# Performance work log

Measured on AMD Instinct MI355X. Metric: run time of the kernel, lower is better.

The kernel has to match this reference:

```python
import jax, jax.numpy as jnp
import numpy as np

B, N, C = 16, 2048, 256  # dim=256, hidden_dim=2*dim -> v,gate each width C
LN_EPS = 1e-5


def setup_inputs() -> dict:
    key = jax.random.key(0)
    ks = jax.random.split(key, 6)
    std = 0.02
    return {
        "x": jax.random.normal(ks[0], (B, N, C), dtype=jnp.float32),
        "H": 64,
        "W": 32,
        "ln_w": jnp.ones((C,), jnp.float32),
        "ln_b": jnp.zeros((C,), jnp.float32),
        "w_hidden": jax.random.normal(ks[1], (C, 2 * C), jnp.float32) * std,
        "b_hidden": jnp.zeros((2 * C,), jnp.float32),
        "w_kv": jax.random.normal(ks[2], (C, C), jnp.float32) * std,  # qkv_bias=False
        "gamma": jnp.ones((2, C), jnp.float32),   # torch.ones(2, dim)
        "beta": jnp.zeros((2, C), jnp.float32),   # torch.zeros(2, dim)
        "w_proj": jax.random.normal(ks[3], (C, C), jnp.float32) * std,
        "b_proj": jnp.zeros((C,), jnp.float32),
    }


def reference(x, H, W, ln_w, ln_b, w_hidden, b_hidden, w_kv, gamma, beta, w_proj, b_proj):
    # H, W are unused by the original forward (pos conv is dead code).
    b, n, c = x.shape
    # LayerNorm
    mu = jnp.mean(x, axis=-1, keepdims=True)
    var = jnp.mean(jnp.square(x - mu), axis=-1, keepdims=True)
    normed = (x - mu) * jax.lax.rsqrt(var + LN_EPS) * ln_w + ln_b
    # to_hidden: Linear + SiLU, then chunk into v, gate (each width c)
    h = jax.nn.silu(normed @ w_hidden + b_hidden)
    v, gate = h[..., :c], h[..., c:]
    # kv projection, then offset-scale into q, k
    Z = normed @ w_kv                                  # (b, n, c)
    QK = Z[..., None, :] * gamma + beta                # (b, n, 2, c)
    q, k = QK[..., 0, :], QK[..., 1, :]
    # relu^2 quadratic attention (no softmax)
    attn = jnp.einsum('bid,bjd->bij', q, k) / n        # (b, n, n)
    A = jnp.square(jax.nn.relu(attn))
    V = jnp.einsum('bij,bjd->bid', A, v)               # (b, n, c)
    # SiLU gating, output projection, residual
    out = (V * gate) @ w_proj + b_proj
    return out + x
```

## Files before the change

kernel.cpp:

```cpp
#include <hip/hip_runtime.h>

#define BN 32768
#define NB 16
#define NN 2048
#define CC 256
#define JT 64
#define NTILES (NN / JT)

using short8  = __attribute__((ext_vector_type(8))) short;
using floatx4 = __attribute__((ext_vector_type(4))) float;

__device__ __forceinline__ unsigned short f2bf(float f) {
  unsigned u = __builtin_bit_cast(unsigned, f);
  u += 0x7fffu + ((u >> 16) & 1u);
  return (unsigned short)(u >> 16);
}
__device__ __forceinline__ float bf2f(unsigned short h) {
  unsigned u = ((unsigned)h) << 16;
  return __builtin_bit_cast(float, u);
}
__device__ __forceinline__ unsigned pk4fp8(float a, float b, float c, float d) {
  unsigned u = __builtin_amdgcn_cvt_pk_fp8_f32(c, d, 0, true);
  return __builtin_amdgcn_cvt_pk_fp8_f32(a, b, (int)u, false);
}
__device__ __forceinline__ long lo64(uint4 v) {
  uint2 t; t.x = v.x; t.y = v.y; return __builtin_bit_cast(long, t);
}
__device__ __forceinline__ long hi64(uint4 v) {
  uint2 t; t.x = v.z; t.y = v.w; return __builtin_bit_cast(long, t);
}
__device__ __forceinline__ void gll16(const void* g, void* l) {
  __builtin_amdgcn_global_load_lds(
      (const __attribute__((address_space(1))) void*)g,
      (__attribute__((address_space(3))) void*)l, 16, 0, 0);
}

__global__ __launch_bounds__(256) void ln_kernel(
    const float* __restrict__ x, const float* __restrict__ lw,
    const float* __restrict__ lb, unsigned short* __restrict__ normed) {
  int row  = blockIdx.x * 4 + (threadIdx.x >> 6);
  int lane = threadIdx.x & 63;
  float4 v = ((const float4*)(x + (size_t)row * CC))[lane];
  float s  = v.x + v.y + v.z + v.w;
  float s2 = v.x * v.x + v.y * v.y + v.z * v.z + v.w * v.w;
#pragma unroll
  for (int off = 32; off; off >>= 1) {
    s  += __shfl_xor(s, off);
    s2 += __shfl_xor(s2, off);
  }
  float mu = s * (1.0f / CC);
  float rs = rsqrtf(s2 * (1.0f / CC) - mu * mu + 1e-5f);
  float4 w = ((const float4*)lw)[lane];
  float4 b = ((const float4*)lb)[lane];
  ushort4 o;
  o.x = f2bf((v.x - mu) * rs * w.x + b.x);
  o.y = f2bf((v.y - mu) * rs * w.y + b.y);
  o.z = f2bf((v.z - mu) * rs * w.z + b.z);
  o.w = f2bf((v.w - mu) * rs * w.w + b.w);
  ((ushort4*)(normed + (size_t)row * CC))[lane] = o;
}

__global__ void wconv_kernel(const float* __restrict__ wh,
                             const float* __restrict__ wkv,
                             const float* __restrict__ wp,
                             unsigned short* __restrict__ wTh,
                             unsigned short* __restrict__ wTkv,
                             unsigned short* __restrict__ wTp) {
  int idx = blockIdx.x * 256 + threadIdx.x;
  if (idx < 131072) {
    int n = idx >> 8, k = idx & 255;
    wTh[idx] = f2bf(wh[(size_t)k * 512 + n]);
  } else if (idx < 196608) {
    int i2 = idx - 131072;
    int n = i2 >> 8, k = i2 & 255;
    wTkv[i2] = f2bf(wkv[(size_t)k * 256 + n]);
  } else {
    int i2 = idx - 196608;
    int n = i2 >> 8, k = i2 & 255;
    wTp[i2] = f2bf(wp[(size_t)k * 256 + n]);
  }
}

__global__ __launch_bounds__(256) void gemm_hidden(
    const unsigned short* __restrict__ A, const unsigned short* __restrict__ BT,
    const float* __restrict__ bias,
    unsigned char* __restrict__ vB, unsigned short* __restrict__ gout) {
  __shared__ unsigned short Al[128 * 256];
  int wave = threadIdx.x >> 6, lane = threadIdx.x & 63;
  int m = lane & 15, g4 = lane >> 4;
  int mb0 = blockIdx.y * 128;
  int nb0 = blockIdx.x * 128;
  const unsigned short* abase = A + (size_t)mb0 * CC;
#pragma unroll
  for (int it = 0; it < 16; ++it) {
    int ci = it * 256 + threadIdx.x;
    int row = ci >> 5, slot = ci & 31;
    gll16(abase + (size_t)row * CC + ((slot ^ (row & 7)) * 8), (char*)Al + ci * 16);
  }
  __syncthreads();
  int m0 = mb0 + (wave & 1) * 64;
  int n0 = nb0 + (wave >> 1) * 64;
  const int mw0 = (wave & 1) * 64;
  floatx4 acc[4][4] = {};
#pragma unroll
  for (int ks = 0; ks < 8; ++ks) {
    short8 af[4], bf[4];
#pragma unroll
    for (int i = 0; i < 4; ++i) {
      int row = mw0 + i * 16 + m;
      int phys = (ks * 4 + g4) ^ (m & 7);
      af[i] = *(const short8*)((const char*)Al + row * 512 + phys * 16);
    }
#pragma unroll
    for (int j = 0; j < 4; ++j)
      bf[j] = *(const short8*)(BT + (size_t)(n0 + j * 16 + m) * CC + ks * 32 + g4 * 8);
#pragma unroll
    for (int i = 0; i < 4; ++i)
#pragma unroll
      for (int j = 0; j < 4; ++j)
        acc[i][j] = __builtin_amdgcn_mfma_f32_16x16x32_bf16(af[i], bf[j], acc[i][j], 0, 0, 0);
  }
  const int sw = (m >> 1) & 3;
  if (nb0 < CC) {
    __syncthreads();
    unsigned char* img = (unsigned char*)Al;
    const int jp4 = (g4 & 1) * 4;
    const int g4h = g4 >> 1;
    const int cw = (wave >> 1) * 64;
    const int jtl = (wave & 1);
#pragma unroll
    for (int j = 0; j < 4; ++j) {
      int cl = cw + j * 16 + m;
      float bv = bias[nb0 + cl];
#pragma unroll
      for (int i = 0; i < 4; ++i) {
        int g4a = ((i * 2 + g4h) & 3) ^ sw;
        int h8 = ((i >> 1) & 1) * 8;
        float s0, s1, s2, s3;
        {
          float h;
          h = acc[i][j][0] + bv; s0 = h / (1.0f + __expf(-h));
          h = acc[i][j][1] + bv; s1 = h / (1.0f + __expf(-h));
          h = acc[i][j][2] + bv; s2 = h / (1.0f + __expf(-h));
          h = acc[i][j][3] + bv; s3 = h / (1.0f + __expf(-h));
        }
        *(unsigned*)(img + jtl * 8192 + cl * 64 + g4a * 16 + h8 + jp4) =
            pk4fp8(s0, s1, s2, s3);
      }
    }
    __syncthreads();
    const size_t tbase = ((size_t)(mb0 >> 11) * 32 + ((mb0 & 2047) >> 6)) * 16384;
#pragma unroll
    for (int it = 0; it < 4; ++it) {
      int o = it * 4096 + threadIdx.x * 16;
      int jl = o >> 13, rem = o & 8191;
      *(uint4*)(vB + tbase + (size_t)jl * 16384 + (size_t)nb0 * 64 + rem) =
          *(const uint4*)(img + o);
    }
  } else {
#pragma unroll
    for (int j = 0; j < 4; ++j) {
      int col = n0 + j * 16 + m;
      float bv = bias[col];
#pragma unroll
      for (int i = 0; i < 4; ++i)
#pragma unroll
        for (int r = 0; r < 4; ++r) {
          int row = m0 + i * 16 + g4 * 4 + r;
          float hh = acc[i][j][r] + bv;
          float sv = hh / (1.0f + __expf(-hh));
          gout[(size_t)row * CC + col - CC] = f2bf(sv);
        }
    }
  }
}

__global__ __launch_bounds__(256) void gemm_kv(
    const unsigned short* __restrict__ A, const unsigned short* __restrict__ BT,
    const float* __restrict__ gamma, const float* __restrict__ beta,
    unsigned char* __restrict__ qout, unsigned char* __restrict__ kout) {
  __shared__ unsigned char kvimg[32768];
  int wave = threadIdx.x >> 6, lane = threadIdx.x & 63;
  int m = lane & 15, g4 = lane >> 4, kb = g4 * 8;
  int m0 = blockIdx.x * 128 + (wave & 1) * 64;
  int n0 = blockIdx.y * 128 + (wave >> 1) * 64;
  floatx4 acc[4][4] = {};
#pragma unroll
  for (int ks = 0; ks < 8; ++ks) {
    short8 af[4], bf[4];
#pragma unroll
    for (int i = 0; i < 4; ++i)
      af[i] = *(const short8*)(A + (size_t)(m0 + i * 16 + m) * CC + ks * 32 + kb);
#pragma unroll
    for (int j = 0; j < 4; ++j)
      bf[j] = *(const short8*)(BT + (size_t)(n0 + j * 16 + m) * CC + ks * 32 + kb);
#pragma unroll
    for (int i = 0; i < 4; ++i)
#pragma unroll
      for (int j = 0; j < 4; ++j)
        acc[i][j] = __builtin_amdgcn_mfma_f32_16x16x32_bf16(bf[j], af[i], acc[i][j], 0, 0, 0);
  }
  const int sw = (m >> 1) & 3;
  unsigned char* qi = kvimg;
  unsigned char* ki = kvimg + 16384;
  const int jbw = (wave & 1) * 4;
  const int ksl = (wave >> 1);
#pragma unroll
  for (int j = 0; j < 4; ++j) {
    int c4 = n0 + j * 16 + g4 * 4;
    float4 g0 = *(const float4*)(gamma + c4);
    float4 b0 = *(const float4*)(beta + c4);
    float4 g1 = *(const float4*)(gamma + CC + c4);
    float4 b1 = *(const float4*)(beta + CC + c4);
    int slot = ((c4 >> 3) & 3) ^ sw;
    int sub = slot * 16 + ((c4 >> 5) & 1) * 8 + (c4 & 7);
    int lbase = ksl * 1024 + m * 64 + sub;
#pragma unroll
    for (int i = 0; i < 4; ++i) {
      int off = (jbw + i) * 2048 + lbase;
      floatx4 z = acc[i][j];
      *(unsigned*)(qi + off) = pk4fp8(z[0] * g0.x + b0.x, z[1] * g0.y + b0.y,
                                      z[2] * g0.z + b0.z, z[3] * g0.w + b0.w);
      *(unsigned*)(ki + off) = pk4fp8(z[0] * g1.x + b1.x, z[1] * g1.y + b1.y,
                                      z[2] * g1.z + b1.z, z[3] * g1.w + b1.w);
    }
  }
  __syncthreads();
  const int mb = blockIdx.x * 128;
  const int jg0 = (mb & 2047) >> 4;
  const int kg0 = blockIdx.y * 2;
  const size_t gbase = ((size_t)(mb >> 11) * 128 + jg0) * 4096;
#pragma unroll
  for (int it = 0; it < 4; ++it) {
    int o = it * 4096 + threadIdx.x * 16;
    int jbl = o >> 11, rem = o & 2047;
    int ks2l = rem >> 10, r2 = rem & 1023;
    size_t gaddr = gbase + (size_t)jbl * 4096 + (size_t)(kg0 + ks2l) * 1024 + r2;
    *(uint4*)(kout + gaddr) = *(const uint4*)(ki + o);
    int n15 = (r2 >> 6) & 15;
    int slot = (r2 >> 4) & 3;
    int os = (o & ~48) | (((slot ^ ((n15 >> 1) & 3)) & 3) << 4);
    *(uint4*)(qout + gaddr) = *(const uint4*)(qi + os);
  }
}

__global__ __launch_bounds__(256, 2) void attn_kernel(
    const unsigned char* __restrict__ qB, const unsigned char* __restrict__ kB,
    const unsigned char* __restrict__ vB, const unsigned short* __restrict__ gg,
    unsigned short* __restrict__ og) {
  __shared__ unsigned char Kl[2][16384];
  __shared__ unsigned char Vl[2][16384];
  const int tid = threadIdx.x;
  const int wave = tid >> 6, lane = tid & 63;
  const int m = lane & 15, g4 = lane >> 4;
  const int id = blockIdx.x;
  const int b = id & 15, bx = id >> 4;
  const int i0 = bx * 64;
  const unsigned char* kimg = kB + (size_t)b * 524288;
  const unsigned char* vimg = vB + (size_t)b * 524288;

  const int iblk = bx * 4 + wave;
  uint4 qf[4];
#pragma unroll
  for (int ks2 = 0; ks2 < 4; ++ks2)
    qf[ks2] = *(const uint4*)(qB + ((size_t)(b * 128 + iblk) * 4 + ks2) * 1024 + m * 64 + g4 * 16);

  floatx4 acc[16] = {};
  const int alo = (m + ((g4 & 1) << 5)) << 2;
  const int ahi = alo + 64;
  const int gsw = (g4 ^ ((m >> 1) & 3)) * 16;

  auto stage = [&](int buf, int t) {
    const unsigned char* kt = kimg + (size_t)t * 16384;
    const unsigned char* vt = vimg + (size_t)t * 16384;
#pragma unroll
    for (int it = 0; it < 4; ++it) {
      int o = (it * 256 + tid) * 16;
      gll16(kt + o, &Kl[buf][o]);
      gll16(vt + o, &Vl[buf][o]);
    }
  };

  stage(0, 0);
  for (int t = 0; t < NTILES; ++t) {
    const int cur = t & 1;
    __syncthreads();
    if (t + 1 < NTILES) stage(cur ^ 1, t + 1);
    floatx4 sacc[4] = {};
#pragma unroll
    for (int ks2 = 0; ks2 < 4; ++ks2) {
#pragma unroll
      for (int jf = 0; jf < 4; ++jf) {
        uint4 kf = *(const uint4*)(&Kl[cur][(jf * 4 + ks2) * 1024 + m * 64 + gsw]);
        sacc[jf] = __builtin_amdgcn_mfma_f32_16x16x32_fp8_fp8(
            lo64(kf), lo64(qf[ks2]), sacc[jf], 0, 0, 0);
        sacc[jf] = __builtin_amdgcn_mfma_f32_16x16x32_fp8_fp8(
            hi64(kf), hi64(qf[ks2]), sacc[jf], 0, 0, 0);
      }
    }
    unsigned pk[4];
#pragma unroll
    for (int jf = 0; jf < 4; ++jf) {
      float p0 = fmaxf(sacc[jf][0], 0.0f) * 0.0625f;
      float p1 = fmaxf(sacc[jf][1], 0.0f) * 0.0625f;
      float p2 = fmaxf(sacc[jf][2], 0.0f) * 0.0625f;
      float p3 = fmaxf(sacc[jf][3], 0.0f) * 0.0625f;
      pk[jf] = pk4fp8(p0 * p0, p1 * p1, p2 * p2, p3 * p3);
    }
    long ap[2];
#pragma unroll
    for (int kk = 0; kk < 2; ++kk) {
      int A0 = __builtin_amdgcn_ds_bpermute(alo, (int)pk[2 * kk]);
      int B0 = __builtin_amdgcn_ds_bpermute(alo, (int)pk[2 * kk + 1]);
      int C0 = __builtin_amdgcn_ds_bpermute(ahi, (int)pk[2 * kk]);
      int D0 = __builtin_amdgcn_ds_bpermute(ahi, (int)pk[2 * kk + 1]);
      unsigned lo = (g4 & 2) ? (unsigned)B0 : (unsigned)A0;
      unsigned hi = (g4 & 2) ? (unsigned)D0 : (unsigned)C0;
      ap[kk] = (long)(((unsigned long long)hi << 32) | lo);
    }
#pragma unroll
    for (int cf = 0; cf < 16; ++cf) {
      uint4 vfr = *(const uint4*)(&Vl[cur][cf * 1024 + m * 64 + gsw]);
      acc[cf] = __builtin_amdgcn_mfma_f32_16x16x32_fp8_fp8(ap[0], lo64(vfr), acc[cf], 0, 0, 0);
      acc[cf] = __builtin_amdgcn_mfma_f32_16x16x32_fp8_fp8(ap[1], hi64(vfr), acc[cf], 0, 0, 0);
    }
  }
  const float sc = 1.0f / 16384.0f;
  const size_t bo = (size_t)b * NN * CC;
#pragma unroll
  for (int cf = 0; cf < 16; ++cf)
#pragma unroll
    for (int r = 0; r < 4; ++r) {
      int row = i0 + wave * 16 + g4 * 4 + r;
      int col = cf * 16 + m;
      size_t off = bo + (size_t)row * CC + col;
      og[off] = f2bf(acc[cf][r] * sc * bf2f(gg[off]));
    }
}

__global__ __launch_bounds__(256) void gemm_proj(
    const unsigned short* __restrict__ A, const unsigned short* __restrict__ BT,
    const float* __restrict__ bias, const float* __restrict__ xres,
    float* __restrict__ out) {
  int wave = threadIdx.x >> 6, lane = threadIdx.x & 63;
  int m = lane & 15, g4 = lane >> 4, kb = g4 * 8;
  int m0 = blockIdx.x * 128 + (wave & 1) * 64;
  int n0 = blockIdx.y * 128 + (wave >> 1) * 64;
  floatx4 acc[4][4] = {};
#pragma unroll
  for (int ks = 0; ks < 8; ++ks) {
    short8 af[4], bf[4];
#pragma unroll
    for (int i = 0; i < 4; ++i)
      af[i] = *(const short8*)(A + (size_t)(m0 + i * 16 + m) * CC + ks * 32 + kb);
#pragma unroll
    for (int j = 0; j < 4; ++j)
      bf[j] = *(const short8*)(BT + (size_t)(n0 + j * 16 + m) * CC + ks * 32 + kb);
#pragma unroll
    for (int i = 0; i < 4; ++i)
#pragma unroll
      for (int j = 0; j < 4; ++j)
        acc[i][j] = __builtin_amdgcn_mfma_f32_16x16x32_bf16(af[i], bf[j], acc[i][j], 0, 0, 0);
  }
#pragma unroll
  for (int j = 0; j < 4; ++j) {
    int col = n0 + j * 16 + m;
    float bv = bias[col];
#pragma unroll
    for (int i = 0; i < 4; ++i)
#pragma unroll
      for (int r = 0; r < 4; ++r) {
        int row = m0 + i * 16 + g4 * 4 + r;
        size_t rr = (size_t)row * CC;
        out[rr + col] = acc[i][j][r] + bv + xres[rr + col];
      }
  }
}

extern "C" void kernel_launch(void* const* d_in, const int* in_sizes, int n_in,
                              void* d_out, int out_size, void* d_ws, size_t ws_size,
                              hipStream_t stream) {
  const float* x        = (const float*)d_in[0];
  const float* ln_w     = (const float*)d_in[3];
  const float* ln_b     = (const float*)d_in[4];
  const float* w_hidden = (const float*)d_in[5];
  const float* b_hidden = (const float*)d_in[6];
  const float* w_kv     = (const float*)d_in[7];
  const float* gamma    = (const float*)d_in[8];
  const float* beta     = (const float*)d_in[9];
  const float* w_proj   = (const float*)d_in[10];
  const float* b_proj   = (const float*)d_in[11];
  float* out = (float*)d_out;
  char* ws = (char*)d_ws;

  const size_t SZ = (size_t)BN * CC * 2;
  const size_t HZ = SZ / 2;
  unsigned short* slot0 = (unsigned short*)(ws);
  unsigned short* gbuf  = (unsigned short*)(ws + SZ);
  unsigned char*  qB    = (unsigned char*)(ws + 2 * SZ);
  unsigned char*  kB    = (unsigned char*)(ws + 2 * SZ + HZ);
  unsigned char*  vB    = (unsigned char*)(ws + 2 * SZ + 2 * HZ);
  unsigned short* wTh   = (unsigned short*)(ws + 2 * SZ + 3 * HZ);
  unsigned short* wTkv  = (unsigned short*)(ws + 2 * SZ + 3 * HZ + 512 * 256 * 2);
  unsigned short* wTp   = (unsigned short*)(ws + 2 * SZ + 3 * HZ + 512 * 256 * 2 + 256 * 256 * 2);

  wconv_kernel<<<1024, 256, 0, stream>>>(w_hidden, w_kv, w_proj, wTh, wTkv, wTp);
  ln_kernel<<<BN / 4, 256, 0, stream>>>(x, ln_w, ln_b, slot0);
  gemm_hidden<<<dim3(4, 256), 256, 0, stream>>>(slot0, wTh, b_hidden, vB, gbuf);
  gemm_kv<<<dim3(BN / 128, 2), 256, 0, stream>>>(slot0, wTkv, gamma, beta, qB, kB);
  attn_kernel<<<512, 256, 0, stream>>>(qB, kB, vB, gbuf, slot0);
  gemm_proj<<<dim3(BN / 128, 2), 256, 0, stream>>>(slot0, wTp, b_proj, x, out);
}
```

Before: 157.0 us.

## Double query rows per attention wave to reuse K/V tiles; tile weight transpose

Each attention wave now handles two 16-row query blocks, so every K and V fragment read from LDS feeds two MFMAs. The block covers 128 query rows, the grid drops to 256 blocks, and occupancy is lowered to one block per SU to leave room for the doubled accumulators. The weight conversion kernel now uses a shared-memory tiled transpose with coalesced float4 reads instead of strided scalar gathers. The risks are a grid of only 256 blocks, which may underfill 256 CUs, and higher register pressure with less latency hiding.

```diff
diff --git a/kernel.cpp b/kernel.cpp
--- a/kernel.cpp
+++ b/kernel.cpp
@@ -60,25 +60,28 @@
   ((ushort4*)(normed + (size_t)row * CC))[lane] = o;
 }
 
-__global__ void wconv_kernel(const float* __restrict__ wh,
-                             const float* __restrict__ wkv,
-                             const float* __restrict__ wp,
-                             unsigned short* __restrict__ wTh,
-                             unsigned short* __restrict__ wTkv,
-                             unsigned short* __restrict__ wTp) {
-  int idx = blockIdx.x * 256 + threadIdx.x;
-  if (idx < 131072) {
-    int n = idx >> 8, k = idx & 255;
-    wTh[idx] = f2bf(wh[(size_t)k * 512 + n]);
-  } else if (idx < 196608) {
-    int i2 = idx - 131072;
-    int n = i2 >> 8, k = i2 & 255;
-    wTkv[i2] = f2bf(wkv[(size_t)k * 256 + n]);
-  } else {
-    int i2 = idx - 196608;
-    int n = i2 >> 8, k = i2 & 255;
-    wTp[i2] = f2bf(wp[(size_t)k * 256 + n]);
-  }
+__global__ __launch_bounds__(256) void wconv_kernel(
+    const float* __restrict__ wh, const float* __restrict__ wkv,
+    const float* __restrict__ wp,
+    unsigned short* __restrict__ wTh, unsigned short* __restrict__ wTkv,
+    unsigned short* __restrict__ wTp) {
+  __shared__ float T[64][65];
+  int bid = blockIdx.x;
+  const float* src; unsigned short* dst; int N, kt, nt;
+  if (bid < 32)      { src = wh;  dst = wTh;  N = 512; kt = bid >> 3;        nt = bid & 7; }
+  else if (bid < 48) { src = wkv; dst = wTkv; N = 256; kt = (bid - 32) >> 2; nt = (bid - 32) & 3; }
+  else               { src = wp;  dst = wTp;  N = 256; kt = (bid - 48) >> 2; nt = (bid - 48) & 3; }
+  int k0 = kt * 64, n0 = nt * 64;
+  int t = threadIdx.x;
+  int r = t >> 2, c0 = (t & 3) * 16;
+#pragma unroll
+  for (int e = 0; e < 4; ++e)
+    *(float4*)(&T[r][c0 + e * 4]) =
+        *(const float4*)(src + (size_t)(k0 + r) * N + n0 + c0 + e * 4);
+  __syncthreads();
+#pragma unroll
+  for (int e = 0; e < 16; ++e)
+    dst[(size_t)(n0 + r) * 256 + k0 + c0 + e] = f2bf(T[c0 + e][r]);
 }
 
 __global__ __launch_bounds__(256) void gemm_hidden(
@@ -244,7 +247,7 @@
   }
 }
 
-__global__ __launch_bounds__(256, 2) void attn_kernel(
+__global__ __launch_bounds__(256, 1) void attn_kernel(
     const unsigned char* __restrict__ qB, const unsigned char* __restrict__ kB,
     const unsigned char* __restrict__ vB, const unsigned short* __restrict__ gg,
     unsigned short* __restrict__ og) {
@@ -255,17 +258,19 @@
   const int m = lane & 15, g4 = lane >> 4;
   const int id = blockIdx.x;
   const int b = id & 15, bx = id >> 4;
-  const int i0 = bx * 64;
+  const int i0 = bx * 128;
   const unsigned char* kimg = kB + (size_t)b * 524288;
   const unsigned char* vimg = vB + (size_t)b * 524288;
 
-  const int iblk = bx * 4 + wave;
-  uint4 qf[4];
-#pragma unroll
-  for (int ks2 = 0; ks2 < 4; ++ks2)
-    qf[ks2] = *(const uint4*)(qB + ((size_t)(b * 128 + iblk) * 4 + ks2) * 1024 + m * 64 + g4 * 16);
-
-  floatx4 acc[16] = {};
+  uint4 qf[2][4];
+#pragma unroll
+  for (int ib = 0; ib < 2; ++ib)
+#pragma unroll
+    for (int ks2 = 0; ks2 < 4; ++ks2)
+      qf[ib][ks2] = *(const uint4*)(qB +
+          ((size_t)(b * 128 + bx * 8 + wave * 2 + ib) * 4 + ks2) * 1024 + m * 64 + g4 * 16);
+
+  floatx4 acc[16][2] = {};
   const int alo = (m + ((g4 & 1) << 5)) << 2;
   const int ahi = alo + 64;
   const int gsw = (g4 ^ ((m >> 1) & 3)) * 16;
@@ -286,43 +291,58 @@
     const int cur = t & 1;
     __syncthreads();
     if (t + 1 < NTILES) stage(cur ^ 1, t + 1);
-    floatx4 sacc[4] = {};
-#pragma unroll
-    for (int ks2 = 0; ks2 < 4; ++ks2) {
-#pragma unroll
-      for (int jf = 0; jf < 4; ++jf) {
-        uint4 kf = *(const uint4*)(&Kl[cur][(jf * 4 + ks2) * 1024 + m * 64 + gsw]);
-        sacc[jf] = __builtin_amdgcn_mfma_f32_16x16x32_fp8_fp8(
-            lo64(kf), lo64(qf[ks2]), sacc[jf], 0, 0, 0);
-        sacc[jf] = __builtin_amdgcn_mfma_f32_16x16x32_fp8_fp8(
-            hi64(kf), hi64(qf[ks2]), sacc[jf], 0, 0, 0);
+    unsigned pk[2][4];
+#pragma unroll
+    for (int jh2 = 0; jh2 < 2; ++jh2) {
+      floatx4 sacc[2][2] = {};
+#pragma unroll
+      for (int ks2 = 0; ks2 < 4; ++ks2)
+#pragma unroll
+        for (int jf2 = 0; jf2 < 2; ++jf2) {
+          int jf = jh2 * 2 + jf2;
+          uint4 kf = *(const uint4*)(&Kl[cur][(jf * 4 + ks2) * 1024 + m * 64 + gsw]);
+          long klo = lo64(kf), khi = hi64(kf);
+#pragma unroll
+          for (int ib = 0; ib < 2; ++ib) {
+            sacc[jf2][ib] = __builtin_amdgcn_mfma_f32_16x16x32_fp8_fp8(
+                klo, lo64(qf[ib][ks2]), sacc[jf2][ib], 0, 0, 0);
+            sacc[jf2][ib] = __builtin_amdgcn_mfma_f32_16x16x32_fp8_fp8(
+                khi, hi64(qf[ib][ks2]), sacc[jf2][ib], 0, 0, 0);
+          }
+        }
+#pragma unroll
+      for (int jf2 = 0; jf2 < 2; ++jf2)
+#pragma unroll
+        for (int ib = 0; ib < 2; ++ib) {
+          float p0 = fmaxf(sacc[jf2][ib][0], 0.0f) * 0.0625f;
+          float p1 = fmaxf(sacc[jf2][ib][1], 0.0f) * 0.0625f;
+          float p2 = fmaxf(sacc[jf2][ib][2], 0.0f) * 0.0625f;
+          float p3 = fmaxf(sacc[jf2][ib][3], 0.0f) * 0.0625f;
+          pk[ib][jh2 * 2 + jf2] = pk4fp8(p0 * p0, p1 * p1, p2 * p2, p3 * p3);
+        }
+    }
+    long ap[2][2];
+#pragma unroll
+    for (int ib = 0; ib < 2; ++ib)
+#pragma unroll
+      for (int kk = 0; kk < 2; ++kk) {
+        int A0 = __builtin_amdgcn_ds_bpermute(alo, (int)pk[ib][2 * kk]);
+        int B0 = __builtin_amdgcn_ds_bpermute(alo, (int)pk[ib][2 * kk + 1]);
+        int C0 = __builtin_amdgcn_ds_bpermute(ahi, (int)pk[ib][2 * kk]);
+        int D0 = __builtin_amdgcn_ds_bpermute(ahi, (int)pk[ib][2 * kk + 1]);
+        unsigned lo = (g4 & 2) ? (unsigned)B0 : (unsigned)A0;
+        unsigned hi = (g4 & 2) ? (unsigned)D0 : (unsigned)C0;
+        ap[ib][kk] = (long)(((unsigned long long)hi << 32) | lo);
       }
-    }
-    unsigned pk[4];
-#pragma unroll
-    for (int jf = 0; jf < 4; ++jf) {
-      float p0 = fmaxf(sacc[jf][0], 0.0f) * 0.0625f;
-      float p1 = fmaxf(sacc[jf][1], 0.0f) * 0.0625f;
-      float p2 = fmaxf(sacc[jf][2], 0.0f) * 0.0625f;
-      float p3 = fmaxf(sacc[jf][3], 0.0f) * 0.0625f;
-      pk[jf] = pk4fp8(p0 * p0, p1 * p1, p2 * p2, p3 * p3);
-    }
-    long ap[2];
-#pragma unroll
-    for (int kk = 0; kk < 2; ++kk) {
-      int A0 = __builtin_amdgcn_ds_bpermute(alo, (int)pk[2 * kk]);
-      int B0 = __builtin_amdgcn_ds_bpermute(alo, (int)pk[2 * kk + 1]);
-      int C0 = __builtin_amdgcn_ds_bpermute(ahi, (int)pk[2 * kk]);
-      int D0 = __builtin_amdgcn_ds_bpermute(ahi, (int)pk[2 * kk + 1]);
-      unsigned lo = (g4 & 2) ? (unsigned)B0 : (unsigned)A0;
-      unsigned hi = (g4 & 2) ? (unsigned)D0 : (unsigned)C0;
-      ap[kk] = (long)(((unsigned long long)hi << 32) | lo);
-    }
 #pragma unroll
     for (int cf = 0; cf < 16; ++cf) {
       uint4 vfr = *(const uint4*)(&Vl[cur][cf * 1024 + m * 64 + gsw]);
-      acc[cf] = __builtin_amdgcn_mfma_f32_16x16x32_fp8_fp8(ap[0], lo64(vfr), acc[cf], 0, 0, 0);
-      acc[cf] = __builtin_amdgcn_mfma_f32_16x16x32_fp8_fp8(ap[1], hi64(vfr), acc[cf], 0, 0, 0);
+      long vlo = lo64(vfr), vhi = hi64(vfr);
+#pragma unroll
+      for (int ib = 0; ib < 2; ++ib) {
+        acc[cf][ib] = __builtin_amdgcn_mfma_f32_16x16x32_fp8_fp8(ap[ib][0], vlo, acc[cf][ib], 0, 0, 0);
+        acc[cf][ib] = __builtin_amdgcn_mfma_f32_16x16x32_fp8_fp8(ap[ib][1], vhi, acc[cf][ib], 0, 0, 0);
+      }
     }
   }
   const float sc = 1.0f / 16384.0f;
@@ -330,12 +350,14 @@
 #pragma unroll
   for (int cf = 0; cf < 16; ++cf)
 #pragma unroll
-    for (int r = 0; r < 4; ++r) {
-      int row = i0 + wave * 16 + g4 * 4 + r;
-      int col = cf * 16 + m;
-      size_t off = bo + (size_t)row * CC + col;
-      og[off] = f2bf(acc[cf][r] * sc * bf2f(gg[off]));
-    }
+    for (int ib = 0; ib < 2; ++ib)
+#pragma unroll
+      for (int r = 0; r < 4; ++r) {
+        int row = i0 + wave * 32 + ib * 16 + g4 * 4 + r;
+        int col = cf * 16 + m;
+        size_t off = bo + (size_t)row * CC + col;
+        og[off] = f2bf(acc[cf][ib][r] * sc * bf2f(gg[off]));
+      }
 }
 
 __global__ __launch_bounds__(256) void gemm_proj(
@@ -404,10 +426,10 @@
   unsigned short* wTkv  = (unsigned short*)(ws + 2 * SZ + 3 * HZ + 512 * 256 * 2);
   unsigned short* wTp   = (unsigned short*)(ws + 2 * SZ + 3 * HZ + 512 * 256 * 2 + 256 * 256 * 2);
 
-  wconv_kernel<<<1024, 256, 0, stream>>>(w_hidden, w_kv, w_proj, wTh, wTkv, wTp);
+  wconv_kernel<<<64, 256, 0, stream>>>(w_hidden, w_kv, w_proj, wTh, wTkv, wTp);
   ln_kernel<<<BN / 4, 256, 0, stream>>>(x, ln_w, ln_b, slot0);
   gemm_hidden<<<dim3(4, 256), 256, 0, stream>>>(slot0, wTh, b_hidden, vB, gbuf);
   gemm_kv<<<dim3(BN / 128, 2), 256, 0, stream>>>(slot0, wTkv, gamma, beta, qB, kB);
-  attn_kernel<<<512, 256, 0, stream>>>(qB, kB, vB, gbuf, slot0);
+  attn_kernel<<<256, 256, 0, stream>>>(qB, kB, vB, gbuf, slot0);
   gemm_proj<<<dim3(BN / 128, 2), 256, 0, stream>>>(slot0, wTp, b_proj, x, out);
 }
```

Measured after the change: 193.1 us. 1.23x slower.

## Split hidden GEMM into v and gate kernels and tile weight transpose through LDS

Applied to the files above, without the earlier changes.

Replaces the strided per-element weight transpose with a 64x64 LDS-tiled transpose that reads coalesced float4 rows, using 64 blocks instead of 1024. Splits the fused hidden GEMM into separate gemm_v and gemm_gate kernels. Both read the A operand straight from global memory instead of staging the whole 128x256 tile in LDS, which cuts LDS use and the load barrier. The cost is an extra kernel launch, and A is now read through uncached-in-LDS global loads, relying on L1/L2 for reuse across the four waves.

```diff
diff --git a/kernel.cpp b/kernel.cpp
--- a/kernel.cpp
+++ b/kernel.cpp
@@ -60,60 +60,50 @@
   ((ushort4*)(normed + (size_t)row * CC))[lane] = o;
 }
 
-__global__ void wconv_kernel(const float* __restrict__ wh,
-                             const float* __restrict__ wkv,
-                             const float* __restrict__ wp,
-                             unsigned short* __restrict__ wTh,
-                             unsigned short* __restrict__ wTkv,
-                             unsigned short* __restrict__ wTp) {
-  int idx = blockIdx.x * 256 + threadIdx.x;
-  if (idx < 131072) {
-    int n = idx >> 8, k = idx & 255;
-    wTh[idx] = f2bf(wh[(size_t)k * 512 + n]);
-  } else if (idx < 196608) {
-    int i2 = idx - 131072;
-    int n = i2 >> 8, k = i2 & 255;
-    wTkv[i2] = f2bf(wkv[(size_t)k * 256 + n]);
-  } else {
-    int i2 = idx - 196608;
-    int n = i2 >> 8, k = i2 & 255;
-    wTp[i2] = f2bf(wp[(size_t)k * 256 + n]);
-  }
-}
-
-__global__ __launch_bounds__(256) void gemm_hidden(
+__global__ __launch_bounds__(256) void wconv_kernel(
+    const float* __restrict__ wh, const float* __restrict__ wkv,
+    const float* __restrict__ wp,
+    unsigned short* __restrict__ wTh, unsigned short* __restrict__ wTkv,
+    unsigned short* __restrict__ wTp) {
+  __shared__ float T[64][65];
+  int bid = blockIdx.x;
+  const float* src; unsigned short* dst; int N, kt, nt;
+  if (bid < 32)      { src = wh;  dst = wTh;  N = 512; kt = bid >> 3;        nt = bid & 7; }
+  else if (bid < 48) { src = wkv; dst = wTkv; N = 256; kt = (bid - 32) >> 2; nt = (bid - 32) & 3; }
+  else               { src = wp;  dst = wTp;  N = 256; kt = (bid - 48) >> 2; nt = (bid - 48) & 3; }
+  int k0 = kt * 64, n0 = nt * 64;
+  int t = threadIdx.x;
+  int r = t >> 2, c0 = (t & 3) * 16;
+#pragma unroll
+  for (int e = 0; e < 4; ++e)
+    *(float4*)(&T[r][c0 + e * 4]) =
+        *(const float4*)(src + (size_t)(k0 + r) * N + n0 + c0 + e * 4);
+  __syncthreads();
+#pragma unroll
+  for (int e = 0; e < 16; ++e)
+    dst[(size_t)(n0 + r) * 256 + k0 + c0 + e] = f2bf(T[c0 + e][r]);
+}
+
+__global__ __launch_bounds__(256) void gemm_v(
     const unsigned short* __restrict__ A, const unsigned short* __restrict__ BT,
-    const float* __restrict__ bias,
-    unsigned char* __restrict__ vB, unsigned short* __restrict__ gout) {
-  __shared__ unsigned short Al[128 * 256];
+    const float* __restrict__ bias, unsigned char* __restrict__ vB) {
+  __shared__ unsigned char img[16384];
   int wave = threadIdx.x >> 6, lane = threadIdx.x & 63;
-  int m = lane & 15, g4 = lane >> 4;
-  int mb0 = blockIdx.y * 128;
-  int nb0 = blockIdx.x * 128;
-  const unsigned short* abase = A + (size_t)mb0 * CC;
-#pragma unroll
-  for (int it = 0; it < 16; ++it) {
-    int ci = it * 256 + threadIdx.x;
-    int row = ci >> 5, slot = ci & 31;
-    gll16(abase + (size_t)row * CC + ((slot ^ (row & 7)) * 8), (char*)Al + ci * 16);
-  }
-  __syncthreads();
-  int m0 = mb0 + (wave & 1) * 64;
-  int n0 = nb0 + (wave >> 1) * 64;
-  const int mw0 = (wave & 1) * 64;
+  int m = lane & 15, g4 = lane >> 4, kb = g4 * 8;
+  int mb = blockIdx.x * 128;
+  int nq = blockIdx.y * 128;
+  int m0 = mb + (wave & 1) * 64;
+  int n0 = nq + (wave >> 1) * 64;
   floatx4 acc[4][4] = {};
 #pragma unroll
   for (int ks = 0; ks < 8; ++ks) {
     short8 af[4], bf[4];
 #pragma unroll
-    for (int i = 0; i < 4; ++i) {
-      int row = mw0 + i * 16 + m;
-      int phys = (ks * 4 + g4) ^ (m & 7);
-      af[i] = *(const short8*)((const char*)Al + row * 512 + phys * 16);
-    }
+    for (int i = 0; i < 4; ++i)
+      af[i] = *(const short8*)(A + (size_t)(m0 + i * 16 + m) * CC + ks * 32 + kb);
 #pragma unroll
     for (int j = 0; j < 4; ++j)
-      bf[j] = *(const short8*)(BT + (size_t)(n0 + j * 16 + m) * CC + ks * 32 + g4 * 8);
+      bf[j] = *(const short8*)(BT + (size_t)(n0 + j * 16 + m) * CC + ks * 32 + kb);
 #pragma unroll
     for (int i = 0; i < 4; ++i)
 #pragma unroll
@@ -121,57 +111,74 @@
         acc[i][j] = __builtin_amdgcn_mfma_f32_16x16x32_bf16(af[i], bf[j], acc[i][j], 0, 0, 0);
   }
   const int sw = (m >> 1) & 3;
-  if (nb0 < CC) {
-    __syncthreads();
-    unsigned char* img = (unsigned char*)Al;
-    const int jp4 = (g4 & 1) * 4;
-    const int g4h = g4 >> 1;
-    const int cw = (wave >> 1) * 64;
-    const int jtl = (wave & 1);
-#pragma unroll
-    for (int j = 0; j < 4; ++j) {
-      int cl = cw + j * 16 + m;
-      float bv = bias[nb0 + cl];
-#pragma unroll
-      for (int i = 0; i < 4; ++i) {
-        int g4a = ((i * 2 + g4h) & 3) ^ sw;
-        int h8 = ((i >> 1) & 1) * 8;
-        float s0, s1, s2, s3;
-        {
-          float h;
-          h = acc[i][j][0] + bv; s0 = h / (1.0f + __expf(-h));
-          h = acc[i][j][1] + bv; s1 = h / (1.0f + __expf(-h));
-          h = acc[i][j][2] + bv; s2 = h / (1.0f + __expf(-h));
-          h = acc[i][j][3] + bv; s3 = h / (1.0f + __expf(-h));
-        }
-        *(unsigned*)(img + jtl * 8192 + cl * 64 + g4a * 16 + h8 + jp4) =
-            pk4fp8(s0, s1, s2, s3);
+  const int jtl = (wave & 1);
+  const int jp4 = (g4 & 1) * 4;
+  const int g4h = g4 >> 1;
+#pragma unroll
+  for (int j = 0; j < 4; ++j) {
+    int col = n0 + j * 16 + m;
+    int cl = col - nq;
+    float bv = bias[col];
+#pragma unroll
+    for (int i = 0; i < 4; ++i) {
+      int g4a = ((i * 2 + g4h) & 3) ^ sw;
+      int h8 = ((i >> 1) & 1) * 8;
+      float h, s0, s1, s2, s3;
+      h = acc[i][j][0] + bv; s0 = h / (1.0f + __expf(-h));
+      h = acc[i][j][1] + bv; s1 = h / (1.0f + __expf(-h));
+      h = acc[i][j][2] + bv; s2 = h / (1.0f + __expf(-h));
+      h = acc[i][j][3] + bv; s3 = h / (1.0f + __expf(-h));
+      *(unsigned*)(img + jtl * 8192 + cl * 64 + g4a * 16 + h8 + jp4) =
+          pk4fp8(s0, s1, s2, s3);
+    }
+  }
+  __syncthreads();
+  const size_t tb = ((size_t)(mb >> 11) * 32 + ((mb & 2047) >> 6)) * 16384;
+#pragma unroll
+  for (int it = 0; it < 4; ++it) {
+    int o = it * 4096 + threadIdx.x * 16;
+    int jl = o >> 13, rem = o & 8191;
+    *(uint4*)(vB + tb + (size_t)jl * 16384 + (size_t)nq * 64 + rem) =
+        *(const uint4*)(img + o);
+  }
+}
+
+__global__ __launch_bounds__(256) void gemm_gate(
+    const unsigned short* __restrict__ A, const unsigned short* __restrict__ BT,
+    const float* __restrict__ bias, unsigned short* __restrict__ gout) {
+  int wave = threadIdx.x >> 6, lane = threadIdx.x & 63;
+  int m = lane & 15, g4 = lane >> 4, kb = g4 * 8;
+  int m0 = blockIdx.x * 128 + (wave & 1) * 64;
+  int n0 = 256 + blockIdx.y * 128 + (wave >> 1) * 64;
+  floatx4 acc[4][4] = {};
+#pragma unroll
+  for (int ks = 0; ks < 8; ++ks) {
+    short8 af[4], bf[4];
+#pragma unroll
+    for (int i = 0; i < 4; ++i)
+      af[i] = *(const short8*)(A + (size_t)(m0 + i * 16 + m) * CC + ks * 32 + kb);
+#pragma unroll
+    for (int j = 0; j < 4; ++j)
+      bf[j] = *(const short8*)(BT + (size_t)(n0 + j * 16 + m) * CC + ks * 32 + kb);
+#pragma unroll
+    for (int i = 0; i < 4; ++i)
+#pragma unroll
+      for (int j = 0; j < 4; ++j)
+        acc[i][j] = __builtin_amdgcn_mfma_f32_16x16x32_bf16(af[i], bf[j], acc[i][j], 0, 0, 0);
+  }
+#pragma unroll
+  for (int j = 0; j < 4; ++j) {
+    int col = n0 + j * 16 + m;
+    float bv = bias[col];
+#pragma unroll
+    for (int i = 0; i < 4; ++i)
+#pragma unroll
+      for (int r = 0; r < 4; ++r) {
+        int row = m0 + i * 16 + g4 * 4 + r;
+        float hh = acc[i][j][r] + bv;
+        float sv = hh / (1.0f + __expf(-hh));
+        gout[(size_t)row * CC + col - 256] = f2bf(sv);
       }
-    }
-    __syncthreads();
-    const size_t tbase = ((size_t)(mb0 >> 11) * 32 + ((mb0 & 2047) >> 6)) * 16384;
-#pragma unroll
-    for (int it = 0; it < 4; ++it) {
-      int o = it * 4096 + threadIdx.x * 16;
-      int jl = o >> 13, rem = o & 8191;
-      *(uint4*)(vB + tbase + (size_t)jl * 16384 + (size_t)nb0 * 64 + rem) =
-          *(const uint4*)(img + o);
-    }
-  } else {
-#pragma unroll
-    for (int j = 0; j < 4; ++j) {
-      int col = n0 + j * 16 + m;
-      float bv = bias[col];
-#pragma unroll
-      for (int i = 0; i < 4; ++i)
-#pragma unroll
-        for (int r = 0; r < 4; ++r) {
-          int row = m0 + i * 16 + g4 * 4 + r;
-          float hh = acc[i][j][r] + bv;
-          float sv = hh / (1.0f + __expf(-hh));
-          gout[(size_t)row * CC + col - CC] = f2bf(sv);
-        }
-    }
   }
 }
 
@@ -404,10 +411,11 @@
   unsigned short* wTkv  = (unsigned short*)(ws + 2 * SZ + 3 * HZ + 512 * 256 * 2);
   unsigned short* wTp   = (unsigned short*)(ws + 2 * SZ + 3 * HZ + 512 * 256 * 2 + 256 * 256 * 2);
 
-  wconv_kernel<<<1024, 256, 0, stream>>>(w_hidden, w_kv, w_proj, wTh, wTkv, wTp);
+  wconv_kernel<<<64, 256, 0, stream>>>(w_hidden, w_kv, w_proj, wTh, wTkv, wTp);
   ln_kernel<<<BN / 4, 256, 0, stream>>>(x, ln_w, ln_b, slot0);
-  gemm_hidden<<<dim3(4, 256), 256, 0, stream>>>(slot0, wTh, b_hidden, vB, gbuf);
   gemm_kv<<<dim3(BN / 128, 2), 256, 0, stream>>>(slot0, wTkv, gamma, beta, qB, kB);
+  gemm_v<<<dim3(BN / 128, 2), 256, 0, stream>>>(slot0, wTh, b_hidden, vB);
+  gemm_gate<<<dim3(BN / 128, 2), 256, 0, stream>>>(slot0, wTh, b_hidden, gbuf);
   attn_kernel<<<512, 256, 0, stream>>>(qB, kB, vB, gbuf, slot0);
   gemm_proj<<<dim3(BN / 128, 2), 256, 0, stream>>>(slot0, wTp, b_proj, x, out);
 }
```

New measurement: 165.3 us. 1.05x slower.
